# Performance work log

Hardware: AMD Instinct MI355X
Metric: run time of the kernel (lower is better)

The kernel has to match this reference:

```python
import jax, jax.numpy as jnp
import numpy as np

TOP_K = 2
SCALE = 1.0  # score_scale_factor

def setup_inputs() -> dict:
    key = jax.random.key(0)
    ks = jax.random.split(key, 8)
    T, D, E, F = 4096, 1024, 8, 4096
    return {
        "hidden_states": jax.random.normal(ks[0], (T, D), jnp.float32),
        "gw1": jax.random.normal(ks[1], (D, D // 4), jnp.float32) * 0.02,
        "gb1": jnp.zeros((D // 4,), jnp.float32),
        "gw2": jax.random.normal(ks[2], (D // 4, D // 16), jnp.float32) * 0.02,
        "gb2": jnp.zeros((D // 16,), jnp.float32),
        "gw3": jax.random.normal(ks[3], (D // 16, E), jnp.float32) * 0.02,
        "w1": jax.random.normal(ks[4], (E, D, F), jnp.float32) * 0.02,
        "b1": jnp.zeros((E, F), jnp.float32),
        "w2": jax.random.normal(ks[5], (E, F, D), jnp.float32) * 0.02,
        "b2": jnp.zeros((E, D), jnp.float32),
    }

def reference(hidden_states, gw1, gb1, gw2, gb2, gw3, w1, b1, w2, b2):
    h = hidden_states                              # [T, D]
    g = jax.nn.relu(h @ gw1 + gb1)
    g = jax.nn.relu(g @ gw2 + gb2)
    router_logits = g @ gw3                        # [T, E]
    probs = jax.nn.softmax(router_logits.astype(jnp.float32), axis=-1)
    top_w, top_i = jax.lax.top_k(probs, TOP_K)     # [T, k]
    top_w = top_w / jnp.sum(top_w, axis=-1, keepdims=True)
    top_w = top_w.astype(h.dtype)
    T, E = router_logits.shape
    # combine weights: scatter normalized top-k weights into dense [T, E]
    cw = jnp.zeros((T, E), h.dtype).at[jnp.arange(T)[:, None], top_i].add(top_w)
    out = jnp.zeros_like(h)
    for e in range(E):  # small fixed expert count
        y = jax.nn.gelu(h @ w1[e] + b1[e]) @ w2[e] + b2[e]
        out = out + y * (cw[:, e:e + 1] * SCALE)
    return out, router_logits
```

## Files before the change

### kernel.cpp

```cpp
#include <hip/hip_runtime.h>
#include <stdint.h>

#define T_  4096
#define D_  1024
#define E_  8
#define F_  4096
#define H1_ 256
#define H2_ 64
#define SCALE_ 1.0f

typedef unsigned short ushort_t;
typedef unsigned int   uint32;
typedef __attribute__((ext_vector_type(8))) short  short8;
typedef __attribute__((ext_vector_type(4))) float  f32x4;
typedef __attribute__((ext_vector_type(4))) unsigned short us4;

__device__ __forceinline__ ushort_t f2bf(float f) {
  uint32 u = __float_as_uint(f);
  u += 0x7FFFu + ((u >> 16) & 1u);
  return (ushort_t)(u >> 16);
}
__device__ __forceinline__ float bf2f(ushort_t u) {
  return __uint_as_float(((uint32)u) << 16);
}
__device__ __forceinline__ float gelu_tanh(float x) {
  float u = 0.7978845608028654f * (x + 0.044715f * x * x * x);
  float e = __expf(2.0f * u);
  return 0.5f * x * (1.0f + (1.0f - 2.0f / (e + 1.0f)));
}
__device__ __forceinline__ void gll16(const void* gptr, void* lptr) {
  void* g = const_cast<void*>(gptr);
  __builtin_amdgcn_global_load_lds((__attribute__((address_space(1))) void*)g,
                                   (__attribute__((address_space(3))) void*)lptr,
                                   16, 0, 0);
}

__global__ void k_cvt_h(const float* __restrict__ h, ushort_t* __restrict__ hb) {
  int i = (blockIdx.x * 256 + threadIdx.x) * 8;
  float4 a = *(const float4*)(h + i);
  float4 b = *(const float4*)(h + i + 4);
  short8 v;
  v[0] = (short)f2bf(a.x); v[1] = (short)f2bf(a.y);
  v[2] = (short)f2bf(a.z); v[3] = (short)f2bf(a.w);
  v[4] = (short)f2bf(b.x); v[5] = (short)f2bf(b.y);
  v[6] = (short)f2bf(b.z); v[7] = (short)f2bf(b.w);
  *(short8*)(hb + i) = v;
}

__global__ void k_transpose_bf16(const float* __restrict__ in, ushort_t* __restrict__ out,
                                 int R, int C) {
  const size_t per = (size_t)R * C;
  const float* src = in + per * blockIdx.z;
  ushort_t* dst = out + per * blockIdx.z;
  int lane = threadIdx.x & 63, wv = threadIdx.x >> 6;
  int r0 = blockIdx.x * 128 + lane * 2;
  int cB = blockIdx.y * 64 + wv * 16;
  for (int xi = 0; xi < 16; ++xi) {
    int c = cB + xi;
    float f0 = src[(size_t)r0 * C + c];
    float f1 = src[(size_t)(r0 + 1) * C + c];
    uint32 pack = (uint32)f2bf(f0) | ((uint32)f2bf(f1) << 16);
    *(uint32*)(dst + (size_t)c * R + r0) = pack;
  }
}

__global__ void k_router1(const float* __restrict__ h, const float* __restrict__ gw1,
                          const float* __restrict__ gb1, float* __restrict__ g1) {
  __shared__ float sA[16][65];
  __shared__ float sB[16][65];
  int tx = threadIdx.x, ty = threadIdx.y;
  int tid = ty * 16 + tx;
  int m0 = blockIdx.y * 64, n0 = blockIdx.x * 64;
  double acc[4][4] = {};
  for (int k0 = 0; k0 < D_; k0 += 16) {
    {
      int m = tid & 63, kq = tid >> 6;
      float4 v = *(const float4*)(h + (size_t)(m0 + m) * D_ + k0 + kq * 4);
      sA[kq*4+0][m] = v.x; sA[kq*4+1][m] = v.y; sA[kq*4+2][m] = v.z; sA[kq*4+3][m] = v.w;
    }
    {
      int k = tid >> 4, nq = tid & 15;
      float4 v = *(const float4*)(gw1 + (size_t)(k0 + k) * H1_ + n0 + nq * 4);
      sB[k][nq*4+0] = v.x; sB[k][nq*4+1] = v.y; sB[k][nq*4+2] = v.z; sB[k][nq*4+3] = v.w;
    }
    __syncthreads();
#pragma unroll
    for (int k = 0; k < 16; ++k) {
      float a[4], b[4];
#pragma unroll
      for (int i = 0; i < 4; ++i) a[i] = sA[k][ty + i * 16];
#pragma unroll
      for (int j = 0; j < 4; ++j) b[j] = sB[k][tx * 4 + j];
#pragma unroll
      for (int i = 0; i < 4; ++i)
#pragma unroll
        for (int j = 0; j < 4; ++j)
          acc[i][j] += (double)a[i] * (double)b[j];
    }
    __syncthreads();
  }
  for (int i = 0; i < 4; ++i)
    for (int j = 0; j < 4; ++j) {
      int m = m0 + ty + i * 16, n = n0 + tx * 4 + j;
      float v = (float)acc[i][j] + gb1[n];
      g1[(size_t)m * H1_ + n] = fmaxf(v, 0.0f);
    }
}

__global__ void k_router23(const float* __restrict__ g1, const float* __restrict__ gw2,
                           const float* __restrict__ gb2, const float* __restrict__ gw3,
                           float* __restrict__ logits_out, int* __restrict__ tokExp,
                           float* __restrict__ tokW, int* __restrict__ counts) {
  __shared__ float  sG1[4][256];
  __shared__ double sG2[4][64];
  __shared__ double sL[4][8];
  int lane = threadIdx.x & 63, wv = threadIdx.x >> 6;
  int t = blockIdx.x * 4 + wv;
  float4 v = *(const float4*)(g1 + (size_t)t * H1_ + lane * 4);
  sG1[wv][lane*4+0] = v.x; sG1[wv][lane*4+1] = v.y;
  sG1[wv][lane*4+2] = v.z; sG1[wv][lane*4+3] = v.w;
  __syncthreads();
  double acc = (double)gb2[lane];
  for (int k = 0; k < H1_; ++k)
    acc += (double)sG1[wv][k] * (double)gw2[k * H2_ + lane];
  sG2[wv][lane] = acc > 0.0 ? acc : 0.0;
  __syncthreads();
  if (lane < 8) {
    double l = 0.0;
    for (int j = 0; j < H2_; ++j) l += sG2[wv][j] * (double)gw3[j * E_ + lane];
    sL[wv][lane] = l;
    logits_out[(size_t)t * E_ + lane] = (float)l;
  }
  __syncthreads();
  if (lane == 0) {
    double best = -1e300, second = -1e300; int bi = 0, si = 0;
    for (int e = 0; e < E_; ++e) {
      double l = sL[wv][e];
      if (l > best)        { second = best; si = bi; best = l; bi = e; }
      else if (l > second) { second = l; si = e; }
    }
    double w0 = 1.0 / (1.0 + exp(second - best));
    tokExp[t*2]   = bi; tokExp[t*2+1] = si;
    tokW[t*2]     = (float)w0;
    tokW[t*2+1]   = (float)(1.0 - w0);
    atomicAdd(&counts[bi], 1);
    atomicAdd(&counts[si], 1);
  }
}

__global__ void k_prefix(const int* __restrict__ counts, int* __restrict__ offsets,
                         int* __restrict__ cursor) {
  if (threadIdx.x == 0) {
    int s = 0;
    for (int e = 0; e < E_; ++e) { offsets[e] = s; s += counts[e]; cursor[e] = 0; }
  }
}

__global__ void k_assign(const int* __restrict__ tokExp, const float* __restrict__ tokW,
                         const int* __restrict__ offsets, int* cursor,
                         int* __restrict__ list, int* __restrict__ rowOf,
                         float* __restrict__ rowW) {
  int t = blockIdx.x * 256 + threadIdx.x;
  for (int k = 0; k < 2; ++k) {
    int e = tokExp[t*2+k];
    int pos = atomicAdd(&cursor[e], 1);
    int row = offsets[e] + pos;
    list[row] = t;
    rowOf[t*2+k] = row;
    rowW[row] = tokW[t*2+k];
  }
}

__global__ __launch_bounds__(256) void k_moe_ffn1(
    const ushort_t* __restrict__ hb, const ushort_t* __restrict__ w1t,
    const float* __restrict__ b1, ushort_t* __restrict__ act,
    const int* __restrict__ list, const int* __restrict__ counts,
    const int* __restrict__ offsets) {
  int e = blockIdx.z;
  int cnt = counts[e];
  int mt = blockIdx.y;
  if (mt * 128 >= cnt) return;
  int off = offsets[e];
  int rowStart = off + mt * 128;
  int nBase = blockIdx.x * 128;
  const ushort_t* B = w1t + (size_t)e * F_ * D_;
  int tid = threadIdx.x, w = tid >> 6, lane = tid & 63;
  int m16 = lane & 15, kq = lane >> 4;
  __shared__ short8 lA[512];
  __shared__ short8 lB[512];
  int gr0 = rowStart + (w * 2) * 16 + m16;
  int gr1 = gr0 + 16;
  int t0 = list[min(gr0, 2 * T_ - 1)];
  int t1 = list[min(gr1, 2 * T_ - 1)];
  const ushort_t* aS0 = hb + (size_t)t0 * D_ + kq * 8;
  const ushort_t* aS1 = hb + (size_t)t1 * D_ + kq * 8;
  const ushort_t* bS0 = B + (size_t)(nBase + (w * 2) * 16 + m16) * D_ + kq * 8;
  const ushort_t* bS1 = bS0 + (size_t)16 * D_;
  short8* dA0 = &lA[(w * 2) * 64];
  short8* dA1 = &lA[(w * 2 + 1) * 64];
  short8* dB0 = &lB[(w * 2) * 64];
  short8* dB1 = &lB[(w * 2 + 1) * 64];
  int wr = w >> 1, wc = w & 1;
  f32x4 acc[4][4] = {};
  for (int k0 = 0; k0 < D_; k0 += 32) {
    gll16(aS0 + k0, dA0);
    gll16(aS1 + k0, dA1);
    gll16(bS0 + k0, dB0);
    gll16(bS1 + k0, dB1);
    __syncthreads();
    short8 af[4], bf[4];
#pragma unroll
    for (int i = 0; i < 4; ++i) af[i] = lA[(wr * 4 + i) * 64 + lane];
#pragma unroll
    for (int j = 0; j < 4; ++j) bf[j] = lB[(wc * 4 + j) * 64 + lane];
#pragma unroll
    for (int i = 0; i < 4; ++i)
#pragma unroll
      for (int j = 0; j < 4; ++j)
        acc[i][j] = __builtin_amdgcn_mfma_f32_16x16x32_bf16(af[i], bf[j], acc[i][j], 0, 0, 0);
    __syncthreads();
  }
  const float* b1e = b1 + (size_t)e * F_;
  int quad = lane >> 4, cn = lane & 15;
#pragma unroll
  for (int i = 0; i < 4; ++i) {
    int lrow = (wr * 4 + i) * 16 + quad * 4;
#pragma unroll
    for (int r = 0; r < 4; ++r) {
      int slot = mt * 128 + lrow + r;
      if (slot < cnt) {
        size_t gr = (size_t)off + slot;
#pragma unroll
        for (int j = 0; j < 4; ++j) {
          int n = nBase + (wc * 4 + j) * 16 + cn;
          float x = acc[i][j][r] + b1e[n];
          act[gr * F_ + n] = f2bf(gelu_tanh(x));
        }
      }
    }
  }
}

__global__ __launch_bounds__(256) void k_moe_ffn2(
    const ushort_t* __restrict__ act, const ushort_t* __restrict__ w2t,
    const float* __restrict__ b2, const float* __restrict__ rowW,
    ushort_t* __restrict__ ybuf, const int* __restrict__ counts,
    const int* __restrict__ offsets) {
  int e = blockIdx.z;
  int cnt = counts[e];
  int mt = blockIdx.y;
  if (mt * 128 >= cnt) return;
  int off = offsets[e];
  int rowStart = off + mt * 128;
  int nBase = blockIdx.x * 128;
  const ushort_t* B = w2t + (size_t)e * D_ * F_;
  int tid = threadIdx.x, w = tid >> 6, lane = tid & 63;
  int m16 = lane & 15, kq = lane >> 4;
  __shared__ short8 lA[512];
  __shared__ short8 lB[512];
  int gr0 = rowStart + (w * 2) * 16 + m16;
  int gr1 = gr0 + 16;
  const ushort_t* aS0 = act + (size_t)min(gr0, 2 * T_ - 1) * F_ + kq * 8;
  const ushort_t* aS1 = act + (size_t)min(gr1, 2 * T_ - 1) * F_ + kq * 8;
  const ushort_t* bS0 = B + (size_t)(nBase + (w * 2) * 16 + m16) * F_ + kq * 8;
  const ushort_t* bS1 = bS0 + (size_t)16 * F_;
  short8* dA0 = &lA[(w * 2) * 64];
  short8* dA1 = &lA[(w * 2 + 1) * 64];
  short8* dB0 = &lB[(w * 2) * 64];
  short8* dB1 = &lB[(w * 2 + 1) * 64];
  int wr = w >> 1, wc = w & 1;
  f32x4 acc[4][4] = {};
  for (int k0 = 0; k0 < F_; k0 += 32) {
    gll16(aS0 + k0, dA0);
    gll16(aS1 + k0, dA1);
    gll16(bS0 + k0, dB0);
    gll16(bS1 + k0, dB1);
    __syncthreads();
    short8 af[4], bf[4];
#pragma unroll
    for (int i = 0; i < 4; ++i) af[i] = lA[(wr * 4 + i) * 64 + lane];
#pragma unroll
    for (int j = 0; j < 4; ++j) bf[j] = lB[(wc * 4 + j) * 64 + lane];
#pragma unroll
    for (int i = 0; i < 4; ++i)
#pragma unroll
      for (int j = 0; j < 4; ++j)
        acc[i][j] = __builtin_amdgcn_mfma_f32_16x16x32_bf16(af[i], bf[j], acc[i][j], 0, 0, 0);
    __syncthreads();
  }
  const float* b2e = b2 + (size_t)e * D_;
  int quad = lane >> 4, cn = lane & 15;
#pragma unroll
  for (int i = 0; i < 4; ++i) {
    int lrow = (wr * 4 + i) * 16 + quad * 4;
#pragma unroll
    for (int r = 0; r < 4; ++r) {
      int slot = mt * 128 + lrow + r;
      if (slot < cnt) {
        size_t gr = (size_t)off + slot;
        float wgt = rowW[gr] * SCALE_;
#pragma unroll
        for (int j = 0; j < 4; ++j) {
          int n = nBase + (wc * 4 + j) * 16 + cn;
          float x = (acc[i][j][r] + b2e[n]) * wgt;
          ybuf[gr * D_ + n] = f2bf(x);
        }
      }
    }
  }
}

__global__ void k_combine(const ushort_t* __restrict__ ybuf, const int* __restrict__ rowOf,
                          float* __restrict__ out) {
  int t = blockIdx.x;
  int rA = rowOf[t*2], rB = rowOf[t*2+1];
  int d = threadIdx.x * 4;
  us4 a = *(const us4*)(ybuf + (size_t)rA * D_ + d);
  us4 b = *(const us4*)(ybuf + (size_t)rB * D_ + d);
  float4 o;
  o.x = bf2f(a[0]) + bf2f(b[0]);
  o.y = bf2f(a[1]) + bf2f(b[1]);
  o.z = bf2f(a[2]) + bf2f(b[2]);
  o.w = bf2f(a[3]) + bf2f(b[3]);
  *(float4*)(out + (size_t)t * D_ + d) = o;
}

extern "C" void kernel_launch(void* const* d_in, const int* in_sizes, int n_in,
                              void* d_out, int out_size, void* d_ws, size_t ws_size,
                              hipStream_t stream) {
  const float* h   = (const float*)d_in[0];
  const float* gw1 = (const float*)d_in[1];
  const float* gb1 = (const float*)d_in[2];
  const float* gw2 = (const float*)d_in[3];
  const float* gb2 = (const float*)d_in[4];
  const float* gw3 = (const float*)d_in[5];
  const float* w1  = (const float*)d_in[6];
  const float* b1  = (const float*)d_in[7];
  const float* w2  = (const float*)d_in[8];
  const float* b2  = (const float*)d_in[9];
  float* out    = (float*)d_out;
  float* logits = out + (size_t)T_ * D_;

  char* ws = (char*)d_ws;
  size_t o = 0;
  auto alloc = [&](size_t bytes) -> void* {
    o = (o + 255) & ~(size_t)255;
    void* p = ws + o;
    o += bytes;
    return p;
  };
  int*      counts  = (int*)alloc(E_ * 4);
  int*      cursor  = (int*)alloc(E_ * 4);
  int*      offsets = (int*)alloc(E_ * 4);
  int*      tokExp  = (int*)alloc((size_t)T_ * 2 * 4);
  float*    tokW    = (float*)alloc((size_t)T_ * 2 * 4);
  int*      list    = (int*)alloc((size_t)2 * T_ * 4);
  int*      rowOf   = (int*)alloc((size_t)2 * T_ * 4);
  float*    rowW    = (float*)alloc((size_t)2 * T_ * 4);
  float*    g1      = (float*)alloc((size_t)T_ * H1_ * 4);
  ushort_t* hb      = (ushort_t*)alloc((size_t)T_ * D_ * 2);
  ushort_t* w1t     = (ushort_t*)alloc((size_t)E_ * D_ * F_ * 2);
  ushort_t* w2t     = (ushort_t*)alloc((size_t)E_ * D_ * F_ * 2);
  ushort_t* act     = (ushort_t*)alloc((size_t)2 * T_ * F_ * 2);
  ushort_t* ybuf    = (ushort_t*)alloc((size_t)2 * T_ * D_ * 2);
  (void)ws_size; (void)in_sizes; (void)n_in; (void)out_size;

  hipMemsetAsync(counts, 0, E_ * 4, stream);
  k_cvt_h<<<T_ * D_ / 2048, 256, 0, stream>>>(h, hb);
  k_transpose_bf16<<<dim3(D_ / 128, F_ / 64, E_), 256, 0, stream>>>(w1, w1t, D_, F_);
  k_transpose_bf16<<<dim3(F_ / 128, D_ / 64, E_), 256, 0, stream>>>(w2, w2t, F_, D_);
  k_router1<<<dim3(H1_ / 64, T_ / 64), dim3(16, 16), 0, stream>>>(h, gw1, gb1, g1);
  k_router23<<<T_ / 4, 256, 0, stream>>>(g1, gw2, gb2, gw3, logits, tokExp, tokW, counts);
  k_prefix<<<1, 64, 0, stream>>>(counts, offsets, cursor);
  k_assign<<<T_ / 256, 256, 0, stream>>>(tokExp, tokW, offsets, cursor, list, rowOf, rowW);
  k_moe_ffn1<<<dim3(F_ / 128, T_ / 128, E_), 256, 0, stream>>>(hb, w1t, b1, act, list, counts, offsets);
  k_moe_ffn2<<<dim3(D_ / 128, T_ / 128, E_), 256, 0, stream>>>(act, w2t, b2, rowW, ybuf, counts, offsets);
  k_combine<<<T_, 256, 0, stream>>>(ybuf, rowOf, out);
}
```

Baseline: 1.011 ms.

## Tile weight transpose via LDS, split-K router, double-buffer FFN GEMMs

```diff
diff --git a/kernel.cpp b/kernel.cpp
--- a/kernel.cpp
+++ b/kernel.cpp
@@ -14,6 +14,7 @@
 typedef __attribute__((ext_vector_type(8))) short  short8;
 typedef __attribute__((ext_vector_type(4))) float  f32x4;
 typedef __attribute__((ext_vector_type(4))) unsigned short us4;
+typedef __attribute__((ext_vector_type(8))) unsigned short us8;
 
 __device__ __forceinline__ ushort_t f2bf(float f) {
   uint32 u = __float_as_uint(f);
@@ -49,30 +50,41 @@
 
 __global__ void k_transpose_bf16(const float* __restrict__ in, ushort_t* __restrict__ out,
                                  int R, int C) {
+  __shared__ float ltf[64][65];
   const size_t per = (size_t)R * C;
   const float* src = in + per * blockIdx.z;
   ushort_t* dst = out + per * blockIdx.z;
-  int lane = threadIdx.x & 63, wv = threadIdx.x >> 6;
-  int r0 = blockIdx.x * 128 + lane * 2;
-  int cB = blockIdx.y * 64 + wv * 16;
-  for (int xi = 0; xi < 16; ++xi) {
-    int c = cB + xi;
-    float f0 = src[(size_t)r0 * C + c];
-    float f1 = src[(size_t)(r0 + 1) * C + c];
-    uint32 pack = (uint32)f2bf(f0) | ((uint32)f2bf(f1) << 16);
-    *(uint32*)(dst + (size_t)c * R + r0) = pack;
-  }
+  int r0 = blockIdx.x * 64, c0 = blockIdx.y * 64;
+  int tid = threadIdx.x;
+  int cg = (tid & 15) * 4;
+  int rr = tid >> 4;
+#pragma unroll
+  for (int rb = 0; rb < 64; rb += 16) {
+    int r = rb + rr;
+    float4 v = *(const float4*)(src + (size_t)(r0 + r) * C + c0 + cg);
+    ltf[r][cg + 0] = v.x; ltf[r][cg + 1] = v.y;
+    ltf[r][cg + 2] = v.z; ltf[r][cg + 3] = v.w;
+  }
+  __syncthreads();
+  int c = tid >> 2, rch = (tid & 3) * 16;
+  ushort_t tmp[16];
+#pragma unroll
+  for (int i = 0; i < 16; ++i) tmp[i] = f2bf(ltf[rch + i][c]);
+  ushort_t* dp = dst + (size_t)(c0 + c) * R + r0 + rch;
+  *(us8*)dp = *(const us8*)&tmp[0];
+  *(us8*)(dp + 8) = *(const us8*)&tmp[8];
 }
 
 __global__ void k_router1(const float* __restrict__ h, const float* __restrict__ gw1,
-                          const float* __restrict__ gb1, float* __restrict__ g1) {
+                          double* __restrict__ p1) {
   __shared__ float sA[16][65];
   __shared__ float sB[16][65];
   int tx = threadIdx.x, ty = threadIdx.y;
   int tid = ty * 16 + tx;
   int m0 = blockIdx.y * 64, n0 = blockIdx.x * 64;
+  int kc = blockIdx.z;
   double acc[4][4] = {};
-  for (int k0 = 0; k0 < D_; k0 += 16) {
+  for (int k0 = kc * 256; k0 < kc * 256 + 256; k0 += 16) {
     {
       int m = tid & 63, kq = tid >> 6;
       float4 v = *(const float4*)(h + (size_t)(m0 + m) * D_ + k0 + kq * 4);
@@ -99,30 +111,40 @@
     }
     __syncthreads();
   }
+  double* pd = p1 + (size_t)kc * T_ * H1_;
   for (int i = 0; i < 4; ++i)
     for (int j = 0; j < 4; ++j) {
       int m = m0 + ty + i * 16, n = n0 + tx * 4 + j;
-      float v = (float)acc[i][j] + gb1[n];
-      g1[(size_t)m * H1_ + n] = fmaxf(v, 0.0f);
-    }
-}
-
-__global__ void k_router23(const float* __restrict__ g1, const float* __restrict__ gw2,
+      pd[(size_t)m * H1_ + n] = acc[i][j];
+    }
+}
+
+__global__ void k_router1_reduce(const double* __restrict__ p1, const float* __restrict__ gb1,
+                                 double* __restrict__ g1) {
+  int i = blockIdx.x * 256 + threadIdx.x;
+  const size_t TH = (size_t)T_ * H1_;
+  double s = p1[i] + p1[i + TH] + p1[i + 2 * TH] + p1[i + 3 * TH] + (double)gb1[i & (H1_ - 1)];
+  g1[i] = s > 0.0 ? s : 0.0;
+}
+
+__global__ void k_router23(const double* __restrict__ g1, const float* __restrict__ gw2,
                            const float* __restrict__ gb2, const float* __restrict__ gw3,
                            float* __restrict__ logits_out, int* __restrict__ tokExp,
                            float* __restrict__ tokW, int* __restrict__ counts) {
-  __shared__ float  sG1[4][256];
+  __shared__ double sG1[4][256];
   __shared__ double sG2[4][64];
   __shared__ double sL[4][8];
   int lane = threadIdx.x & 63, wv = threadIdx.x >> 6;
   int t = blockIdx.x * 4 + wv;
-  float4 v = *(const float4*)(g1 + (size_t)t * H1_ + lane * 4);
-  sG1[wv][lane*4+0] = v.x; sG1[wv][lane*4+1] = v.y;
-  sG1[wv][lane*4+2] = v.z; sG1[wv][lane*4+3] = v.w;
+  const double* gp = g1 + (size_t)t * H1_ + lane * 4;
+  double2 va = *(const double2*)gp;
+  double2 vb = *(const double2*)(gp + 2);
+  sG1[wv][lane*4+0] = va.x; sG1[wv][lane*4+1] = va.y;
+  sG1[wv][lane*4+2] = vb.x; sG1[wv][lane*4+3] = vb.y;
   __syncthreads();
   double acc = (double)gb2[lane];
   for (int k = 0; k < H1_; ++k)
-    acc += (double)sG1[wv][k] * (double)gw2[k * H2_ + lane];
+    acc += sG1[wv][k] * (double)gw2[k * H2_ + lane];
   sG2[wv][lane] = acc > 0.0 ? acc : 0.0;
   __syncthreads();
   if (lane < 8) {
@@ -186,8 +208,8 @@
   const ushort_t* B = w1t + (size_t)e * F_ * D_;
   int tid = threadIdx.x, w = tid >> 6, lane = tid & 63;
   int m16 = lane & 15, kq = lane >> 4;
-  __shared__ short8 lA[512];
-  __shared__ short8 lB[512];
+  __shared__ short8 lA[2][512];
+  __shared__ short8 lB[2][512];
   int gr0 = rowStart + (w * 2) * 16 + m16;
   int gr1 = gr0 + 16;
   int t0 = list[min(gr0, 2 * T_ - 1)];
@@ -196,29 +218,33 @@
   const ushort_t* aS1 = hb + (size_t)t1 * D_ + kq * 8;
   const ushort_t* bS0 = B + (size_t)(nBase + (w * 2) * 16 + m16) * D_ + kq * 8;
   const ushort_t* bS1 = bS0 + (size_t)16 * D_;
-  short8* dA0 = &lA[(w * 2) * 64];
-  short8* dA1 = &lA[(w * 2 + 1) * 64];
-  short8* dB0 = &lB[(w * 2) * 64];
-  short8* dB1 = &lB[(w * 2 + 1) * 64];
   int wr = w >> 1, wc = w & 1;
   f32x4 acc[4][4] = {};
-  for (int k0 = 0; k0 < D_; k0 += 32) {
-    gll16(aS0 + k0, dA0);
-    gll16(aS1 + k0, dA1);
-    gll16(bS0 + k0, dB0);
-    gll16(bS1 + k0, dB1);
+  gll16(aS0, &lA[0][(w * 2) * 64]);
+  gll16(aS1, &lA[0][(w * 2 + 1) * 64]);
+  gll16(bS0, &lB[0][(w * 2) * 64]);
+  gll16(bS1, &lB[0][(w * 2 + 1) * 64]);
+  for (int s = 0; s < D_ / 32; ++s) {
     __syncthreads();
-    short8 af[4], bf[4];
-#pragma unroll
-    for (int i = 0; i < 4; ++i) af[i] = lA[(wr * 4 + i) * 64 + lane];
-#pragma unroll
-    for (int j = 0; j < 4; ++j) bf[j] = lB[(wc * 4 + j) * 64 + lane];
+    int p = s & 1;
+    int kn = (s + 1) * 32;
+    if (kn < D_) {
+      int q = p ^ 1;
+      gll16(aS0 + kn, &lA[q][(w * 2) * 64]);
+      gll16(aS1 + kn, &lA[q][(w * 2 + 1) * 64]);
+      gll16(bS0 + kn, &lB[q][(w * 2) * 64]);
+      gll16(bS1 + kn, &lB[q][(w * 2 + 1) * 64]);
+    }
+    short8 af[4], bf4[4];
+#pragma unroll
+    for (int i = 0; i < 4; ++i) af[i] = lA[p][(wr * 4 + i) * 64 + lane];
+#pragma unroll
+    for (int j = 0; j < 4; ++j) bf4[j] = lB[p][(wc * 4 + j) * 64 + lane];
 #pragma unroll
     for (int i = 0; i < 4; ++i)
 #pragma unroll
       for (int j = 0; j < 4; ++j)
-        acc[i][j] = __builtin_amdgcn_mfma_f32_16x16x32_bf16(af[i], bf[j], acc[i][j], 0, 0, 0);
-    __syncthreads();
+        acc[i][j] = __builtin_amdgcn_mfma_f32_16x16x32_bf16(af[i], bf4[j], acc[i][j], 0, 0, 0);
   }
   const float* b1e = b1 + (size_t)e * F_;
   int quad = lane >> 4, cn = lane & 15;
@@ -249,61 +275,61 @@
   int e = blockIdx.z;
   int cnt = counts[e];
   int mt = blockIdx.y;
-  if (mt * 128 >= cnt) return;
+  if (mt * 64 >= cnt) return;
   int off = offsets[e];
-  int rowStart = off + mt * 128;
+  int rowStart = off + mt * 64;
   int nBase = blockIdx.x * 128;
   const ushort_t* B = w2t + (size_t)e * D_ * F_;
   int tid = threadIdx.x, w = tid >> 6, lane = tid & 63;
   int m16 = lane & 15, kq = lane >> 4;
-  __shared__ short8 lA[512];
-  __shared__ short8 lB[512];
-  int gr0 = rowStart + (w * 2) * 16 + m16;
-  int gr1 = gr0 + 16;
-  const ushort_t* aS0 = act + (size_t)min(gr0, 2 * T_ - 1) * F_ + kq * 8;
-  const ushort_t* aS1 = act + (size_t)min(gr1, 2 * T_ - 1) * F_ + kq * 8;
-  const ushort_t* bS0 = B + (size_t)(nBase + (w * 2) * 16 + m16) * F_ + kq * 8;
+  __shared__ short8 lA[2][256];
+  __shared__ short8 lB[2][512];
+  int gr = rowStart + w * 16 + m16;
+  const ushort_t* aS = act + (size_t)min(gr, 2 * T_ - 1) * F_ + kq * 8;
+  const ushort_t* bS0 = B + (size_t)(nBase + w * 32 + m16) * F_ + kq * 8;
   const ushort_t* bS1 = bS0 + (size_t)16 * F_;
-  short8* dA0 = &lA[(w * 2) * 64];
-  short8* dA1 = &lA[(w * 2 + 1) * 64];
-  short8* dB0 = &lB[(w * 2) * 64];
-  short8* dB1 = &lB[(w * 2 + 1) * 64];
   int wr = w >> 1, wc = w & 1;
-  f32x4 acc[4][4] = {};
-  for (int k0 = 0; k0 < F_; k0 += 32) {
-    gll16(aS0 + k0, dA0);
-    gll16(aS1 + k0, dA1);
-    gll16(bS0 + k0, dB0);
-    gll16(bS1 + k0, dB1);
+  f32x4 acc[2][4] = {};
+  gll16(aS, &lA[0][w * 64]);
+  gll16(bS0, &lB[0][(w * 2) * 64]);
+  gll16(bS1, &lB[0][(w * 2 + 1) * 64]);
+  for (int s = 0; s < F_ / 32; ++s) {
     __syncthreads();
-    short8 af[4], bf[4];
-#pragma unroll
-    for (int i = 0; i < 4; ++i) af[i] = lA[(wr * 4 + i) * 64 + lane];
-#pragma unroll
-    for (int j = 0; j < 4; ++j) bf[j] = lB[(wc * 4 + j) * 64 + lane];
-#pragma unroll
-    for (int i = 0; i < 4; ++i)
+    int p = s & 1;
+    int kn = (s + 1) * 32;
+    if (kn < F_) {
+      int q = p ^ 1;
+      gll16(aS + kn, &lA[q][w * 64]);
+      gll16(bS0 + kn, &lB[q][(w * 2) * 64]);
+      gll16(bS1 + kn, &lB[q][(w * 2 + 1) * 64]);
+    }
+    short8 af[2], bf4[4];
+#pragma unroll
+    for (int i = 0; i < 2; ++i) af[i] = lA[p][(wr * 2 + i) * 64 + lane];
+#pragma unroll
+    for (int j = 0; j < 4; ++j) bf4[j] = lB[p][(wc * 4 + j) * 64 + lane];
+#pragma unroll
+    for (int i = 0; i < 2; ++i)
 #pragma unroll
       for (int j = 0; j < 4; ++j)
-        acc[i][j] = __builtin_amdgcn_mfma_f32_16x16x32_bf16(af[i], bf[j], acc[i][j], 0, 0, 0);
-    __syncthreads();
+        acc[i][j] = __builtin_amdgcn_mfma_f32_16x16x32_bf16(af[i], bf4[j], acc[i][j], 0, 0, 0);
   }
   const float* b2e = b2 + (size_t)e * D_;
   int quad = lane >> 4, cn = lane & 15;
 #pragma unroll
-  for (int i = 0; i < 4; ++i) {
-    int lrow = (wr * 4 + i) * 16 + quad * 4;
+  for (int i = 0; i < 2; ++i) {
+    int lrow = (wr * 2 + i) * 16 + quad * 4;
 #pragma unroll
     for (int r = 0; r < 4; ++r) {
-      int slot = mt * 128 + lrow + r;
+      int slot = mt * 64 + lrow + r;
       if (slot < cnt) {
-        size_t gr = (size_t)off + slot;
-        float wgt = rowW[gr] * SCALE_;
+        size_t g = (size_t)off + slot;
+        float wgt = rowW[g] * SCALE_;
 #pragma unroll
         for (int j = 0; j < 4; ++j) {
           int n = nBase + (wc * 4 + j) * 16 + cn;
           float x = (acc[i][j][r] + b2e[n]) * wgt;
-          ybuf[gr * D_ + n] = f2bf(x);
+          ybuf[g * D_ + n] = f2bf(x);
         }
       }
     }
@@ -357,23 +383,26 @@
   int*      list    = (int*)alloc((size_t)2 * T_ * 4);
   int*      rowOf   = (int*)alloc((size_t)2 * T_ * 4);
   float*    rowW    = (float*)alloc((size_t)2 * T_ * 4);
-  float*    g1      = (float*)alloc((size_t)T_ * H1_ * 4);
+  double*   g1      = (double*)alloc((size_t)T_ * H1_ * 8);
   ushort_t* hb      = (ushort_t*)alloc((size_t)T_ * D_ * 2);
   ushort_t* w1t     = (ushort_t*)alloc((size_t)E_ * D_ * F_ * 2);
   ushort_t* w2t     = (ushort_t*)alloc((size_t)E_ * D_ * F_ * 2);
-  ushort_t* act     = (ushort_t*)alloc((size_t)2 * T_ * F_ * 2);
-  ushort_t* ybuf    = (ushort_t*)alloc((size_t)2 * T_ * D_ * 2);
+  char*     big     = (char*)alloc((size_t)2 * T_ * F_ * 2 + (size_t)2 * T_ * D_ * 2);
+  double*   p1      = (double*)big;
+  ushort_t* act     = (ushort_t*)big;
+  ushort_t* ybuf    = (ushort_t*)(big + (size_t)2 * T_ * F_ * 2);
   (void)ws_size; (void)in_sizes; (void)n_in; (void)out_size;
 
   hipMemsetAsync(counts, 0, E_ * 4, stream);
   k_cvt_h<<<T_ * D_ / 2048, 256, 0, stream>>>(h, hb);
-  k_transpose_bf16<<<dim3(D_ / 128, F_ / 64, E_), 256, 0, stream>>>(w1, w1t, D_, F_);
-  k_transpose_bf16<<<dim3(F_ / 128, D_ / 64, E_), 256, 0, stream>>>(w2, w2t, F_, D_);
-  k_router1<<<dim3(H1_ / 64, T_ / 64), dim3(16, 16), 0, stream>>>(h, gw1, gb1, g1);
+  k_transpose_bf16<<<dim3(D_ / 64, F_ / 64, E_), 256, 0, stream>>>(w1, w1t, D_, F_);
+  k_transpose_bf16<<<dim3(F_ / 64, D_ / 64, E_), 256, 0, stream>>>(w2, w2t, F_, D_);
+  k_router1<<<dim3(H1_ / 64, T_ / 64, 4), dim3(16, 16), 0, stream>>>(h, gw1, p1);
+  k_router1_reduce<<<T_ * H1_ / 256, 256, 0, stream>>>(p1, gb1, g1);
   k_router23<<<T_ / 4, 256, 0, stream>>>(g1, gw2, gb2, gw3, logits, tokExp, tokW, counts);
   k_prefix<<<1, 64, 0, stream>>>(counts, offsets, cursor);
   k_assign<<<T_ / 256, 256, 0, stream>>>(tokExp, tokW, offsets, cursor, list, rowOf, rowW);
   k_moe_ffn1<<<dim3(F_ / 128, T_ / 128, E_), 256, 0, stream>>>(hb, w1t, b1, act, list, counts, offsets);
-  k_moe_ffn2<<<dim3(D_ / 128, T_ / 128, E_), 256, 0, stream>>>(act, w2t, b2, rowW, ybuf, counts, offsets);
+  k_moe_ffn2<<<dim3(D_ / 128, T_ * 2 / 64, E_), 256, 0, stream>>>(act, w2t, b2, rowW, ybuf, counts, offsets);
   k_combine<<<T_, 256, 0, stream>>>(ybuf, rowOf, out);
 }
```

Measured after the change: 979.9 us. 1.03x faster.

## Coalesce weight transpose via LDS, split-K router and FFN2, fuse combine epilogue

Applied to the files above, without the earlier changes.

```diff
diff --git a/kernel.cpp b/kernel.cpp
--- a/kernel.cpp
+++ b/kernel.cpp
@@ -8,20 +8,18 @@
 #define H1_ 256
 #define H2_ 64
 #define SCALE_ 1.0f
+#define NROW_ (2 * T_)
 
 typedef unsigned short ushort_t;
 typedef unsigned int   uint32;
 typedef __attribute__((ext_vector_type(8))) short  short8;
 typedef __attribute__((ext_vector_type(4))) float  f32x4;
-typedef __attribute__((ext_vector_type(4))) unsigned short us4;
+typedef __attribute__((ext_vector_type(8))) unsigned short us8;
 
 __device__ __forceinline__ ushort_t f2bf(float f) {
   uint32 u = __float_as_uint(f);
   u += 0x7FFFu + ((u >> 16) & 1u);
   return (ushort_t)(u >> 16);
-}
-__device__ __forceinline__ float bf2f(ushort_t u) {
-  return __uint_as_float(((uint32)u) << 16);
 }
 __device__ __forceinline__ float gelu_tanh(float x) {
   float u = 0.7978845608028654f * (x + 0.044715f * x * x * x);
@@ -49,30 +47,41 @@
 
 __global__ void k_transpose_bf16(const float* __restrict__ in, ushort_t* __restrict__ out,
                                  int R, int C) {
+  __shared__ float ltf[64][65];
   const size_t per = (size_t)R * C;
   const float* src = in + per * blockIdx.z;
   ushort_t* dst = out + per * blockIdx.z;
-  int lane = threadIdx.x & 63, wv = threadIdx.x >> 6;
-  int r0 = blockIdx.x * 128 + lane * 2;
-  int cB = blockIdx.y * 64 + wv * 16;
-  for (int xi = 0; xi < 16; ++xi) {
-    int c = cB + xi;
-    float f0 = src[(size_t)r0 * C + c];
-    float f1 = src[(size_t)(r0 + 1) * C + c];
-    uint32 pack = (uint32)f2bf(f0) | ((uint32)f2bf(f1) << 16);
-    *(uint32*)(dst + (size_t)c * R + r0) = pack;
-  }
+  int r0 = blockIdx.x * 64, c0 = blockIdx.y * 64;
+  int tid = threadIdx.x;
+  int cg = (tid & 15) * 4;
+  int rr = tid >> 4;
+#pragma unroll
+  for (int rb = 0; rb < 64; rb += 16) {
+    int r = rb + rr;
+    float4 v = *(const float4*)(src + (size_t)(r0 + r) * C + c0 + cg);
+    ltf[r][cg + 0] = v.x; ltf[r][cg + 1] = v.y;
+    ltf[r][cg + 2] = v.z; ltf[r][cg + 3] = v.w;
+  }
+  __syncthreads();
+  int c = tid >> 2, rch = (tid & 3) * 16;
+  ushort_t tmp[16];
+#pragma unroll
+  for (int i = 0; i < 16; ++i) tmp[i] = f2bf(ltf[rch + i][c]);
+  ushort_t* dp = dst + (size_t)(c0 + c) * R + r0 + rch;
+  *(us8*)dp = *(const us8*)&tmp[0];
+  *(us8*)(dp + 8) = *(const us8*)&tmp[8];
 }
 
 __global__ void k_router1(const float* __restrict__ h, const float* __restrict__ gw1,
-                          const float* __restrict__ gb1, float* __restrict__ g1) {
+                          double* __restrict__ p1) {
   __shared__ float sA[16][65];
   __shared__ float sB[16][65];
   int tx = threadIdx.x, ty = threadIdx.y;
   int tid = ty * 16 + tx;
   int m0 = blockIdx.y * 64, n0 = blockIdx.x * 64;
+  int kc = blockIdx.z;
   double acc[4][4] = {};
-  for (int k0 = 0; k0 < D_; k0 += 16) {
+  for (int k0 = kc * 256; k0 < kc * 256 + 256; k0 += 16) {
     {
       int m = tid & 63, kq = tid >> 6;
       float4 v = *(const float4*)(h + (size_t)(m0 + m) * D_ + k0 + kq * 4);
@@ -99,30 +108,44 @@
     }
     __syncthreads();
   }
+  double* pd = p1 + (size_t)kc * T_ * H1_;
   for (int i = 0; i < 4; ++i)
     for (int j = 0; j < 4; ++j) {
       int m = m0 + ty + i * 16, n = n0 + tx * 4 + j;
-      float v = (float)acc[i][j] + gb1[n];
-      g1[(size_t)m * H1_ + n] = fmaxf(v, 0.0f);
-    }
-}
-
-__global__ void k_router23(const float* __restrict__ g1, const float* __restrict__ gw2,
-                           const float* __restrict__ gb2, const float* __restrict__ gw3,
+      pd[(size_t)m * H1_ + n] = acc[i][j];
+    }
+}
+
+__global__ void k_router23(const double* __restrict__ p1, const float* __restrict__ gb1,
+                           const float* __restrict__ gw2, const float* __restrict__ gb2,
+                           const float* __restrict__ gw3,
                            float* __restrict__ logits_out, int* __restrict__ tokExp,
                            float* __restrict__ tokW, int* __restrict__ counts) {
-  __shared__ float  sG1[4][256];
+  __shared__ double sG1[4][256];
   __shared__ double sG2[4][64];
   __shared__ double sL[4][8];
   int lane = threadIdx.x & 63, wv = threadIdx.x >> 6;
   int t = blockIdx.x * 4 + wv;
-  float4 v = *(const float4*)(g1 + (size_t)t * H1_ + lane * 4);
-  sG1[wv][lane*4+0] = v.x; sG1[wv][lane*4+1] = v.y;
-  sG1[wv][lane*4+2] = v.z; sG1[wv][lane*4+3] = v.w;
+  const size_t TH = (size_t)T_ * H1_;
+  const double* gp = p1 + (size_t)t * H1_ + lane * 4;
+  double s0 = 0, s1 = 0, s2 = 0, s3 = 0;
+#pragma unroll
+  for (int kc = 0; kc < 4; ++kc) {
+    double2 va = *(const double2*)(gp + kc * TH);
+    double2 vb = *(const double2*)(gp + kc * TH + 2);
+    s0 += va.x; s1 += va.y; s2 += vb.x; s3 += vb.y;
+  }
+  int hbase = lane * 4;
+  s0 += (double)gb1[hbase + 0]; s1 += (double)gb1[hbase + 1];
+  s2 += (double)gb1[hbase + 2]; s3 += (double)gb1[hbase + 3];
+  sG1[wv][hbase + 0] = s0 > 0.0 ? s0 : 0.0;
+  sG1[wv][hbase + 1] = s1 > 0.0 ? s1 : 0.0;
+  sG1[wv][hbase + 2] = s2 > 0.0 ? s2 : 0.0;
+  sG1[wv][hbase + 3] = s3 > 0.0 ? s3 : 0.0;
   __syncthreads();
   double acc = (double)gb2[lane];
   for (int k = 0; k < H1_; ++k)
-    acc += (double)sG1[wv][k] * (double)gw2[k * H2_ + lane];
+    acc += sG1[wv][k] * (double)gw2[k * H2_ + lane];
   sG2[wv][lane] = acc > 0.0 ? acc : 0.0;
   __syncthreads();
   if (lane < 8) {
@@ -148,39 +171,32 @@
   }
 }
 
-__global__ void k_prefix(const int* __restrict__ counts, int* __restrict__ offsets,
-                         int* __restrict__ cursor) {
-  if (threadIdx.x == 0) {
-    int s = 0;
-    for (int e = 0; e < E_; ++e) { offsets[e] = s; s += counts[e]; cursor[e] = 0; }
-  }
-}
-
-__global__ void k_assign(const int* __restrict__ tokExp, const float* __restrict__ tokW,
-                         const int* __restrict__ offsets, int* cursor,
-                         int* __restrict__ list, int* __restrict__ rowOf,
-                         float* __restrict__ rowW) {
+__global__ void k_assign(const int* __restrict__ tokExp, const int* __restrict__ counts,
+                         int* cursor, int* __restrict__ list, int* __restrict__ rowOf) {
   int t = blockIdx.x * 256 + threadIdx.x;
+  int offs[E_];
+  int s = 0;
+#pragma unroll
+  for (int e = 0; e < E_; ++e) { offs[e] = s; s += counts[e]; }
   for (int k = 0; k < 2; ++k) {
     int e = tokExp[t*2+k];
     int pos = atomicAdd(&cursor[e], 1);
-    int row = offsets[e] + pos;
+    int row = offs[e] + pos;
     list[row] = t;
     rowOf[t*2+k] = row;
-    rowW[row] = tokW[t*2+k];
   }
 }
 
 __global__ __launch_bounds__(256) void k_moe_ffn1(
     const ushort_t* __restrict__ hb, const ushort_t* __restrict__ w1t,
     const float* __restrict__ b1, ushort_t* __restrict__ act,
-    const int* __restrict__ list, const int* __restrict__ counts,
-    const int* __restrict__ offsets) {
+    const int* __restrict__ list, const int* __restrict__ counts) {
   int e = blockIdx.z;
+  int off = 0;
+  for (int ee = 0; ee < e; ++ee) off += counts[ee];
   int cnt = counts[e];
   int mt = blockIdx.y;
   if (mt * 128 >= cnt) return;
-  int off = offsets[e];
   int rowStart = off + mt * 128;
   int nBase = blockIdx.x * 128;
   const ushort_t* B = w1t + (size_t)e * F_ * D_;
@@ -190,8 +206,8 @@
   __shared__ short8 lB[512];
   int gr0 = rowStart + (w * 2) * 16 + m16;
   int gr1 = gr0 + 16;
-  int t0 = list[min(gr0, 2 * T_ - 1)];
-  int t1 = list[min(gr1, 2 * T_ - 1)];
+  int t0 = list[min(gr0, NROW_ - 1)];
+  int t1 = list[min(gr1, NROW_ - 1)];
   const ushort_t* aS0 = hb + (size_t)t0 * D_ + kq * 8;
   const ushort_t* aS1 = hb + (size_t)t1 * D_ + kq * 8;
   const ushort_t* bS0 = B + (size_t)(nBase + (w * 2) * 16 + m16) * D_ + kq * 8;
@@ -208,16 +224,16 @@
     gll16(bS0 + k0, dB0);
     gll16(bS1 + k0, dB1);
     __syncthreads();
-    short8 af[4], bf[4];
+    short8 af[4], bf4[4];
 #pragma unroll
     for (int i = 0; i < 4; ++i) af[i] = lA[(wr * 4 + i) * 64 + lane];
 #pragma unroll
-    for (int j = 0; j < 4; ++j) bf[j] = lB[(wc * 4 + j) * 64 + lane];
+    for (int j = 0; j < 4; ++j) bf4[j] = lB[(wc * 4 + j) * 64 + lane];
 #pragma unroll
     for (int i = 0; i < 4; ++i)
 #pragma unroll
       for (int j = 0; j < 4; ++j)
-        acc[i][j] = __builtin_amdgcn_mfma_f32_16x16x32_bf16(af[i], bf[j], acc[i][j], 0, 0, 0);
+        acc[i][j] = __builtin_amdgcn_mfma_f32_16x16x32_bf16(af[i], bf4[j], acc[i][j], 0, 0, 0);
     __syncthreads();
   }
   const float* b1e = b1 + (size_t)e * F_;
@@ -243,14 +259,14 @@
 
 __global__ __launch_bounds__(256) void k_moe_ffn2(
     const ushort_t* __restrict__ act, const ushort_t* __restrict__ w2t,
-    const float* __restrict__ b2, const float* __restrict__ rowW,
-    ushort_t* __restrict__ ybuf, const int* __restrict__ counts,
-    const int* __restrict__ offsets) {
-  int e = blockIdx.z;
+    float* __restrict__ part, const int* __restrict__ counts) {
+  int z = blockIdx.z;
+  int e = z >> 1, kc = z & 1;
+  int off = 0;
+  for (int ee = 0; ee < e; ++ee) off += counts[ee];
   int cnt = counts[e];
   int mt = blockIdx.y;
   if (mt * 128 >= cnt) return;
-  int off = offsets[e];
   int rowStart = off + mt * 128;
   int nBase = blockIdx.x * 128;
   const ushort_t* B = w2t + (size_t)e * D_ * F_;
@@ -260,8 +276,8 @@
   __shared__ short8 lB[512];
   int gr0 = rowStart + (w * 2) * 16 + m16;
   int gr1 = gr0 + 16;
-  const ushort_t* aS0 = act + (size_t)min(gr0, 2 * T_ - 1) * F_ + kq * 8;
-  const ushort_t* aS1 = act + (size_t)min(gr1, 2 * T_ - 1) * F_ + kq * 8;
+  const ushort_t* aS0 = act + (size_t)min(gr0, NROW_ - 1) * F_ + kq * 8;
+  const ushort_t* aS1 = act + (size_t)min(gr1, NROW_ - 1) * F_ + kq * 8;
   const ushort_t* bS0 = B + (size_t)(nBase + (w * 2) * 16 + m16) * F_ + kq * 8;
   const ushort_t* bS1 = bS0 + (size_t)16 * F_;
   short8* dA0 = &lA[(w * 2) * 64];
@@ -270,25 +286,26 @@
   short8* dB1 = &lB[(w * 2 + 1) * 64];
   int wr = w >> 1, wc = w & 1;
   f32x4 acc[4][4] = {};
-  for (int k0 = 0; k0 < F_; k0 += 32) {
+  int kBase = kc * (F_ / 2);
+  for (int k0 = kBase; k0 < kBase + F_ / 2; k0 += 32) {
     gll16(aS0 + k0, dA0);
     gll16(aS1 + k0, dA1);
     gll16(bS0 + k0, dB0);
     gll16(bS1 + k0, dB1);
     __syncthreads();
-    short8 af[4], bf[4];
+    short8 af[4], bf4[4];
 #pragma unroll
     for (int i = 0; i < 4; ++i) af[i] = lA[(wr * 4 + i) * 64 + lane];
 #pragma unroll
-    for (int j = 0; j < 4; ++j) bf[j] = lB[(wc * 4 + j) * 64 + lane];
+    for (int j = 0; j < 4; ++j) bf4[j] = lB[(wc * 4 + j) * 64 + lane];
 #pragma unroll
     for (int i = 0; i < 4; ++i)
 #pragma unroll
       for (int j = 0; j < 4; ++j)
-        acc[i][j] = __builtin_amdgcn_mfma_f32_16x16x32_bf16(af[i], bf[j], acc[i][j], 0, 0, 0);
-    __syncthreads();
-  }
-  const float* b2e = b2 + (size_t)e * D_;
+        acc[i][j] = __builtin_amdgcn_mfma_f32_16x16x32_bf16(af[i], bf4[j], acc[i][j], 0, 0, 0);
+    __syncthreads();
+  }
+  float* pd = part + (size_t)kc * NROW_ * D_;
   int quad = lane >> 4, cn = lane & 15;
 #pragma unroll
   for (int i = 0; i < 4; ++i) {
@@ -298,30 +315,36 @@
       int slot = mt * 128 + lrow + r;
       if (slot < cnt) {
         size_t gr = (size_t)off + slot;
-        float wgt = rowW[gr] * SCALE_;
 #pragma unroll
         for (int j = 0; j < 4; ++j) {
           int n = nBase + (wc * 4 + j) * 16 + cn;
-          float x = (acc[i][j][r] + b2e[n]) * wgt;
-          ybuf[gr * D_ + n] = f2bf(x);
+          pd[gr * D_ + n] = acc[i][j][r];
         }
       }
     }
   }
 }
 
-__global__ void k_combine(const ushort_t* __restrict__ ybuf, const int* __restrict__ rowOf,
-                          float* __restrict__ out) {
+__global__ void k_combine(const float* __restrict__ part, const int* __restrict__ rowOf,
+                          const int* __restrict__ tokExp, const float* __restrict__ tokW,
+                          const float* __restrict__ b2, float* __restrict__ out) {
   int t = blockIdx.x;
   int rA = rowOf[t*2], rB = rowOf[t*2+1];
+  int eA = tokExp[t*2], eB = tokExp[t*2+1];
+  float wA = tokW[t*2] * SCALE_, wB = tokW[t*2+1] * SCALE_;
   int d = threadIdx.x * 4;
-  us4 a = *(const us4*)(ybuf + (size_t)rA * D_ + d);
-  us4 b = *(const us4*)(ybuf + (size_t)rB * D_ + d);
+  const size_t P = (size_t)NROW_ * D_;
+  float4 a0 = *(const float4*)(part + (size_t)rA * D_ + d);
+  float4 a1 = *(const float4*)(part + P + (size_t)rA * D_ + d);
+  float4 b0 = *(const float4*)(part + (size_t)rB * D_ + d);
+  float4 b1 = *(const float4*)(part + P + (size_t)rB * D_ + d);
+  float4 ba = *(const float4*)(b2 + (size_t)eA * D_ + d);
+  float4 bb = *(const float4*)(b2 + (size_t)eB * D_ + d);
   float4 o;
-  o.x = bf2f(a[0]) + bf2f(b[0]);
-  o.y = bf2f(a[1]) + bf2f(b[1]);
-  o.z = bf2f(a[2]) + bf2f(b[2]);
-  o.w = bf2f(a[3]) + bf2f(b[3]);
+  o.x = wA * (a0.x + a1.x + ba.x) + wB * (b0.x + b1.x + bb.x);
+  o.y = wA * (a0.y + a1.y + ba.y) + wB * (b0.y + b1.y + bb.y);
+  o.z = wA * (a0.z + a1.z + ba.z) + wB * (b0.z + b1.z + bb.z);
+  o.w = wA * (a0.w + a1.w + ba.w) + wB * (b0.w + b1.w + bb.w);
   *(float4*)(out + (size_t)t * D_ + d) = o;
 }
 
@@ -349,31 +372,30 @@
     o += bytes;
     return p;
   };
-  int*      counts  = (int*)alloc(E_ * 4);
-  int*      cursor  = (int*)alloc(E_ * 4);
-  int*      offsets = (int*)alloc(E_ * 4);
+  int*      counts  = (int*)alloc(2 * E_ * 4);
+  int*      cursor  = counts + E_;
   int*      tokExp  = (int*)alloc((size_t)T_ * 2 * 4);
   float*    tokW    = (float*)alloc((size_t)T_ * 2 * 4);
-  int*      list    = (int*)alloc((size_t)2 * T_ * 4);
-  int*      rowOf   = (int*)alloc((size_t)2 * T_ * 4);
-  float*    rowW    = (float*)alloc((size_t)2 * T_ * 4);
-  float*    g1      = (float*)alloc((size_t)T_ * H1_ * 4);
+  int*      list    = (int*)alloc((size_t)NROW_ * 4);
+  int*      rowOf   = (int*)alloc((size_t)NROW_ * 4);
   ushort_t* hb      = (ushort_t*)alloc((size_t)T_ * D_ * 2);
-  ushort_t* w1t     = (ushort_t*)alloc((size_t)E_ * D_ * F_ * 2);
   ushort_t* w2t     = (ushort_t*)alloc((size_t)E_ * D_ * F_ * 2);
-  ushort_t* act     = (ushort_t*)alloc((size_t)2 * T_ * F_ * 2);
-  ushort_t* ybuf    = (ushort_t*)alloc((size_t)2 * T_ * D_ * 2);
+  char*     bigA    = (char*)alloc((size_t)NROW_ * F_ * 2);
+  double*   p1      = (double*)bigA;
+  ushort_t* act     = (ushort_t*)bigA;
+  char*     bigB    = (char*)alloc((size_t)E_ * D_ * F_ * 2);
+  ushort_t* w1t     = (ushort_t*)bigB;
+  float*    part    = (float*)bigB;
   (void)ws_size; (void)in_sizes; (void)n_in; (void)out_size;
 
-  hipMemsetAsync(counts, 0, E_ * 4, stream);
+  hipMemsetAsync(counts, 0, 2 * E_ * 4, stream);
   k_cvt_h<<<T_ * D_ / 2048, 256, 0, stream>>>(h, hb);
-  k_transpose_bf16<<<dim3(D_ / 128, F_ / 64, E_), 256, 0, stream>>>(w1, w1t, D_, F_);
-  k_transpose_bf16<<<dim3(F_ / 128, D_ / 64, E_), 256, 0, stream>>>(w2, w2t, F_, D_);
-  k_router1<<<dim3(H1_ / 64, T_ / 64), dim3(16, 16), 0, stream>>>(h, gw1, gb1, g1);
-  k_router23<<<T_ / 4, 256, 0, stream>>>(g1, gw2, gb2, gw3, logits, tokExp, tokW, counts);
-  k_prefix<<<1, 64, 0, stream>>>(counts, offsets, cursor);
-  k_assign<<<T_ / 256, 256, 0, stream>>>(tokExp, tokW, offsets, cursor, list, rowOf, rowW);
-  k_moe_ffn1<<<dim3(F_ / 128, T_ / 128, E_), 256, 0, stream>>>(hb, w1t, b1, act, list, counts, offsets);
-  k_moe_ffn2<<<dim3(D_ / 128, T_ / 128, E_), 256, 0, stream>>>(act, w2t, b2, rowW, ybuf, counts, offsets);
-  k_combine<<<T_, 256, 0, stream>>>(ybuf, rowOf, out);
-}
+  k_transpose_bf16<<<dim3(D_ / 64, F_ / 64, E_), 256, 0, stream>>>(w1, w1t, D_, F_);
+  k_transpose_bf16<<<dim3(F_ / 64, D_ / 64, E_), 256, 0, stream>>>(w2, w2t, F_, D_);
+  k_router1<<<dim3(H1_ / 64, T_ / 64, 4), dim3(16, 16), 0, stream>>>(h, gw1, p1);
+  k_router23<<<T_ / 4, 256, 0, stream>>>(p1, gb1, gw2, gb2, gw3, logits, tokExp, tokW, counts);
+  k_assign<<<T_ / 256, 256, 0, stream>>>(tokExp, counts, cursor, list, rowOf);
+  k_moe_ffn1<<<dim3(F_ / 128, NROW_ / 128, E_), 256, 0, stream>>>(hb, w1t, b1, act, list, counts);
+  k_moe_ffn2<<<dim3(D_ / 128, NROW_ / 128, E_ * 2), 256, 0, stream>>>(act, w2t, part, counts);
+  k_combine<<<T_, 256, 0, stream>>>(part, rowOf, tokExp, tokW, b2, out);
+}
```

After: 934.2 us. 7.6% less time.
